# Performance work log

Measured on AMD Instinct MI355X. Metric: run time of the kernel, lower is better.

The kernel has to match this reference:

```python
import jax, jax.numpy as jnp
import numpy as np

B, S, D, H, DFF = 2, 2048, 768, 12, 3072
DK = D // H
EPS = 1e-6
NEG = -1e9


def setup_inputs() -> dict:
    key = jax.random.key(0)
    ks = jax.random.split(key, 16)
    s = 1.0 / np.sqrt(D)
    inp = {
        'x': jax.random.normal(ks[0], (B, S, D), jnp.float32),
        'wq': jax.random.normal(ks[1], (D, D), jnp.float32) * s,
        'bq': jnp.zeros((D,), jnp.float32),
        'wk': jax.random.normal(ks[2], (D, D), jnp.float32) * s,
        'bk': jnp.zeros((D,), jnp.float32),
        'wv': jax.random.normal(ks[3], (D, D), jnp.float32) * s,
        'bv': jnp.zeros((D,), jnp.float32),
        'wo': jax.random.normal(ks[4], (D, D), jnp.float32) * s,
        'bo': jnp.zeros((D,), jnp.float32),
        'w1': jax.random.normal(ks[5], (D, DFF), jnp.float32) * s,
        'b1': jnp.zeros((DFF,), jnp.float32),
        'w2': jax.random.normal(ks[6], (DFF, D), jnp.float32) * (1.0 / np.sqrt(DFF)),
        'b2': jnp.zeros((D,), jnp.float32),
        'alpha1': jnp.ones((1,), jnp.float32),
        'beta1': jnp.zeros((1,), jnp.float32),
        'alpha2': jnp.ones((1,), jnp.float32),
        'beta2': jnp.zeros((1,), jnp.float32),
        'mask': jax.random.randint(ks[7], (1, 1, S, S), 0, 2, jnp.int32),
    }
    return inp


def layernorm(x, alpha, beta):
    # torch: mean and UNBIASED std (ddof=1), eps added to std (not variance)
    mean = jnp.mean(x, axis=-1, keepdims=True)
    std = jnp.std(x, axis=-1, keepdims=True, ddof=1)
    return alpha * (x - mean) / (std + EPS) + beta


def encoder_layer(x, wq, bq, wk, bk, wv, bv, wo, bo, w1, b1, w2, b2,
                  alpha1, beta1, alpha2, beta2, mask):
    # projections -> [B, H, S, DK]
    def split_heads(t):
        return t.reshape(B, S, H, DK).transpose(0, 2, 1, 3)
    q = split_heads(x @ wq + bq)
    k = split_heads(x @ wk + bk)
    v = split_heads(x @ wv + bv)
    scores = jnp.einsum('bhqd,bhkd->bhqk', q, k) / np.sqrt(DK)  # [B,H,S,S]
    scores = jnp.where(mask == 0, NEG, scores)
    attn = jax.nn.softmax(scores, axis=-1)
    ctx = jnp.einsum('bhqk,bhkd->bhqd', attn, v)
    ctx = ctx.transpose(0, 2, 1, 3).reshape(B, S, D)
    attn_out = ctx @ wo + bo
    x = layernorm(x + attn_out, alpha1, beta1)
    ff = jax.nn.relu(x @ w1 + b1) @ w2 + b2
    x = layernorm(x + ff, alpha2, beta2)
    return x


def reference(x, wq, bq, wk, bk, wv, bv, wo, bo, w1, b1, w2, b2,
              alpha1, beta1, alpha2, beta2, mask):
    return encoder_layer(x, wq, bq, wk, bk, wv, bv, wo, bo, w1, b1, w2, b2,
                         alpha1, beta1, alpha2, beta2, mask)
```

## Files before the change

### kernel.cpp

```cpp
#include <hip/hip_runtime.h>
#include <hip/hip_bf16.h>


typedef short short8 __attribute__((ext_vector_type(8)));
typedef float floatx4 __attribute__((ext_vector_type(4)));
typedef unsigned short ushort_t;
typedef ushort_t ushort4_t __attribute__((ext_vector_type(4)));

#define B_ 2
#define S_ 2048
#define D_ 768
#define H_ 12
#define DK_ 64
#define DFF_ 3072
#define M_ (B_ * S_)
#define RS_ (3 * D_)

#define LOG2E 1.44269504f
#define FMAX_SHIFT 16.0f

__device__ __forceinline__ float bf2f(ushort_t h) {
  union { unsigned int u; float f; } v; v.u = ((unsigned int)h) << 16; return v.f;
}
__device__ __forceinline__ ushort_t f2bf(float f) {
  union { float f; unsigned int u; } v; v.f = f;
  unsigned int u = v.u;
  unsigned int r = (u + 0x7fffu + ((u >> 16) & 1u)) >> 16;
  return (ushort_t)r;
}

__global__ __launch_bounds__(256) void transpose_f2b(
    const float* __restrict__ in, ushort_t* __restrict__ out, int K, int N) {
  __shared__ ushort_t t[32][33];
  const int nt = blockIdx.x * 32, kt = blockIdx.y * 32;
  const int tx = threadIdx.x, ty = threadIdx.y;
#pragma unroll
  for (int i = 0; i < 4; i++)
    t[ty + i * 8][tx] = f2bf(in[(size_t)(kt + ty + i * 8) * N + nt + tx]);
  __syncthreads();
#pragma unroll
  for (int i = 0; i < 4; i++)
    out[(size_t)(nt + ty + i * 8) * K + kt + tx] = t[tx][ty + i * 8];
}

__global__ __launch_bounds__(256) void transpose4_f2b(
    const float* __restrict__ wq, const float* __restrict__ wk,
    const float* __restrict__ wv, const float* __restrict__ wo,
    ushort_t* __restrict__ wTqkv, ushort_t* __restrict__ woT) {
  __shared__ ushort_t t[32][33];
  const int z = blockIdx.z;
  const float* in = (z == 0) ? wq : (z == 1) ? wk : (z == 2) ? wv : wo;
  ushort_t* out = (z < 3) ? (wTqkv + (size_t)z * D_ * D_) : woT;
  const int nt = blockIdx.x * 32, kt = blockIdx.y * 32;
  const int tx = threadIdx.x, ty = threadIdx.y;
#pragma unroll
  for (int i = 0; i < 4; i++)
    t[ty + i * 8][tx] = f2bf(in[(size_t)(kt + ty + i * 8) * D_ + nt + tx]);
  __syncthreads();
#pragma unroll
  for (int i = 0; i < 4; i++)
    out[(size_t)(nt + ty + i * 8) * D_ + kt + tx] = t[tx][ty + i * 8];
}

__global__ __launch_bounds__(256) void mask_to_biasp(
    const int* __restrict__ mask, ushort_t* __restrict__ out) {
  const int t = blockIdx.x * 256 + threadIdx.x;
  const int q = t >> 8;
  const int cc = t & 255;
  const int k0 = (cc >> 3) * 64;
  const int g = cc & 7, f = g >> 2, lq = g & 3;
  const int* mrow = mask + (size_t)q * S_ + k0;
  const ushort_t cm = f2bf(-1.4427e9f);
  const ushort_t cu = f2bf(-FMAX_SHIFT * LOG2E);
  short8 o;
#pragma unroll
  for (int n2 = 0; n2 < 2; n2++)
#pragma unroll
    for (int r = 0; r < 4; r++) {
      const int kpl = 32 * f + 16 * n2 + 4 * lq + r;
      o[n2 * 4 + r] = (short)((mrow[kpl] == 0) ? cm : cu);
    }
  *(short8*)(out + (size_t)q * S_ + k0 + g * 8) = o;
}

__global__ __launch_bounds__(256) void vtrans(
    const ushort_t* __restrict__ qkv, ushort_t* __restrict__ vt) {
  __shared__ __align__(16) ushort_t T[64 * 72];
  const int tid = threadIdx.x;
  const int bh = blockIdx.y, b = bh / H_, h = bh % H_;
  const int k0 = blockIdx.x * 64;
  const ushort_t* vbase = qkv + (size_t)(b * S_) * RS_ + 2 * D_ + h * DK_;
#pragma unroll
  for (int i = 0; i < 2; i++) {
    const int idx = tid + i * 256;
    const int r = idx >> 3, c = idx & 7;
    short8 vv = *(const short8*)(vbase + (size_t)(k0 + r) * RS_ + c * 8);
    const int sw = (r >> 3) ^ c;
#pragma unroll
    for (int j = 0; j < 8; j++)
      T[(c * 8 + j) * 72 + sw * 8 + (r & 7)] = (ushort_t)vv[j];
  }
  __syncthreads();
#pragma unroll
  for (int i = 0; i < 2; i++) {
    const int ch = tid + i * 256;
    const int d = ch >> 3, g = ch & 7, f = g >> 2, lq = g & 3;
    short8 o;
#pragma unroll
    for (int n2 = 0; n2 < 2; n2++)
#pragma unroll
      for (int r = 0; r < 4; r++) {
        const int kpl = 32 * f + 16 * n2 + 4 * lq + r;
        o[n2 * 4 + r] = (short)T[d * 72 + (((kpl >> 3) ^ (d >> 3)) * 8) + (kpl & 7)];
      }
    *(short8*)(vt + ((size_t)bh * 64 + d) * S_ + k0 + g * 8) = o;
  }
}

__global__ __launch_bounds__(256) void cvt_f2b(
    const float* __restrict__ in, ushort_t* __restrict__ out, int n) {
  const int i = (blockIdx.x * 256 + threadIdx.x) * 4;
  if (i >= n) return;
#pragma unroll
  for (int j = 0; j < 4; j++) out[i + j] = f2bf(in[i + j]);
}

__global__ void concat3(const float* __restrict__ a, const float* __restrict__ b,
                        const float* __restrict__ c, float* __restrict__ o, int n) {
  int i = blockIdx.x * 256 + threadIdx.x;
  if (i >= 3 * n) return;
  o[i] = (i < n) ? a[i] : (i < 2 * n ? b[i - n] : c[i - 2 * n]);
}

template <int BN>
__global__ __launch_bounds__(256) void gemm_bt_t(
    const ushort_t* __restrict__ A, const ushort_t* __restrict__ Bt,
    const float* __restrict__ bias, ushort_t* __restrict__ C,
    int M, int N, int K, int relu, int qcols, float qscale) {
  constexpr int WN = (BN == 128) ? 2 : 1;
  constexpr int WM = 4 / WN;
  constexpr int FI = 128 / WM / 16;
  constexpr int FJ = BN / WN / 16;
  __shared__ __align__(16) ushort_t Al[128 * 32];
  __shared__ __align__(16) ushort_t Bl[BN * 32];
  const int tid = threadIdx.x;
  const int w = tid >> 6, lane = tid & 63;
  const int wm = (WN == 2) ? (w >> 1) : w;
  const int wn = (WN == 2) ? (w & 1) : 0;
  const int lq = lane >> 4, lr = lane & 15;
  const int m0 = blockIdx.y * 128, n0 = blockIdx.x * BN;

  floatx4 acc[FI][FJ];
#pragma unroll
  for (int i = 0; i < FI; i++)
#pragma unroll
    for (int j = 0; j < FJ; j++) acc[i][j] = (floatx4){0.f, 0.f, 0.f, 0.f};

  for (int k0 = 0; k0 < K; k0 += 32) {
    __syncthreads();
#pragma unroll
    for (int i = 0; i < 2; i++) {
      const int base = (w * 2 + i) * 512;
      const int e = base + lane * 8;
      const int row = e >> 5, col = e & 31;
      __builtin_amdgcn_global_load_lds(
          (const __attribute__((address_space(1))) void*)(A + (size_t)(m0 + row) * K + k0 + col),
          (__attribute__((address_space(3))) void*)(&Al[base]), 16, 0, 0);
    }
#pragma unroll
    for (int i = 0; i < BN / 64; i++) {
      const int base = (w * (BN / 64) + i) * 512;
      const int e = base + lane * 8;
      const int row = e >> 5, col = e & 31;
      __builtin_amdgcn_global_load_lds(
          (const __attribute__((address_space(1))) void*)(Bt + (size_t)(n0 + row) * K + k0 + col),
          (__attribute__((address_space(3))) void*)(&Bl[base]), 16, 0, 0);
    }
    __syncthreads();

    short8 af[FI], bf[FJ];
#pragma unroll
    for (int i = 0; i < FI; i++)
      af[i] = *(const short8*)&Al[(wm * (FI * 16) + i * 16 + lr) * 32 + lq * 8];
#pragma unroll
    for (int j = 0; j < FJ; j++)
      bf[j] = *(const short8*)&Bl[(wn * (FJ * 16) + j * 16 + lr) * 32 + lq * 8];
#pragma unroll
    for (int i = 0; i < FI; i++)
#pragma unroll
      for (int j = 0; j < FJ; j++)
        acc[i][j] = __builtin_amdgcn_mfma_f32_16x16x32_bf16(af[i], bf[j], acc[i][j], 0, 0, 0);
  }

#pragma unroll
  for (int i = 0; i < FI; i++) {
    const int m = m0 + wm * (FI * 16) + i * 16 + lq * 4;
#pragma unroll
    for (int j = 0; j < FJ; j++) {
      const int n = n0 + wn * (FJ * 16) + j * 16 + lr;
      const float bv = bias[n];
#pragma unroll
      for (int r = 0; r < 4; r++) {
        float v = acc[i][j][r] + bv;
        if (n < qcols) v *= qscale;
        if (relu) v = v > 0.f ? v : 0.f;
        C[(size_t)(m + r) * N + n] = f2bf(v);
      }
    }
  }
}

__global__ __launch_bounds__(256, 3) void flash_attn(
    const ushort_t* __restrict__ qkv, const ushort_t* __restrict__ vt,
    const ushort_t* __restrict__ maskp, ushort_t* __restrict__ ctx) {
  __shared__ __align__(16) ushort_t lds[2][3][64 * 64];
  const int tid = threadIdx.x;
  const int w = tid >> 6, lane = tid & 63;
  const int lq = lane >> 4, lr = lane & 15;
  const int blk = blockIdx.x;
  const int bh = blk >> 5, qb = blk & 31;
  const int b = bh / H_, h = bh % H_;
  const int q0 = qb * 64;
  const ushort_t* qbase = qkv + (size_t)(b * S_) * RS_ + h * DK_;
  const ushort_t* kbase = qbase + D_;
  const ushort_t* vtb   = vt + (size_t)bh * DK_ * S_;
  const ushort_t* mb    = maskp + (size_t)q0 * S_;

  short8 qfr[2];
#pragma unroll
  for (int f = 0; f < 2; f++)
    qfr[f] = *(const short8*)(
        qbase + (size_t)(q0 + w * 16 + lr) * RS_ + f * 32 + lq * 8);

  auto stage = [&](int k0, int s) {
#pragma unroll
    for (int i = 0; i < 2; i++) {
      const int id = i * 256 + tid;
      const int row = id >> 3;
      const int cc = ((id & 7) ^ (row & 7)) * 8;
      const int dbase = (i * 256 + w * 64) * 8;
      __builtin_amdgcn_global_load_lds(
          (const __attribute__((address_space(1))) void*)(kbase + (size_t)(k0 + row) * RS_ + cc),
          (__attribute__((address_space(3))) void*)(&lds[s][0][dbase]), 16, 0, 0);
      __builtin_amdgcn_global_load_lds(
          (const __attribute__((address_space(1))) void*)(vtb + (size_t)row * S_ + k0 + cc),
          (__attribute__((address_space(3))) void*)(&lds[s][1][dbase]), 16, 0, 0);
      __builtin_amdgcn_global_load_lds(
          (const __attribute__((address_space(1))) void*)(mb + (size_t)row * S_ + k0 + cc),
          (__attribute__((address_space(3))) void*)(&lds[s][2][dbase]), 16, 0, 0);
    }
  };

  floatx4 oacc[4];
#pragma unroll
  for (int dt = 0; dt < 4; dt++) oacc[dt] = (floatx4){0.f, 0.f, 0.f, 0.f};
  float li = 0.f;

  stage(0, 0);
  __syncthreads();

  const int sw8 = lr & 7;
  const int c0 = (lq ^ sw8) * 8;
  const int c1 = ((4 + lq) ^ sw8) * 8;

  for (int t = 0; t < S_ / 64; t++) {
    const int s = t & 1;
    stage((t + 1) * 64, s ^ 1);

    const ushort_t* kl = &lds[s][0][0];
    const ushort_t* vl = &lds[s][1][0];
    const ushort_t* ml = &lds[s][2][0];

    const int mrow = (w * 16 + lr) * 64;
    short8 bb0 = *(const short8*)(ml + mrow + c0);
    short8 bb1 = *(const short8*)(ml + mrow + c1);

    floatx4 sacc[4];
#pragma unroll
    for (int n = 0; n < 4; n++) sacc[n] = (floatx4){0.f, 0.f, 0.f, 0.f};
#pragma unroll
    for (int n = 0; n < 4; n++) {
      const int krow = (n * 16 + lr) * 64;
      short8 a0 = *(const short8*)(kl + krow + c0);
      short8 a1 = *(const short8*)(kl + krow + c1);
      sacc[n] = __builtin_amdgcn_mfma_f32_16x16x32_bf16(a0, qfr[0], sacc[n], 0, 0, 0);
      sacc[n] = __builtin_amdgcn_mfma_f32_16x16x32_bf16(a1, qfr[1], sacc[n], 0, 0, 0);
    }

    short8 pf[2];
#pragma unroll
    for (int f = 0; f < 2; f++) {
      const short8 bb = f ? bb1 : bb0;
      union { __hip_bfloat162 h2[4]; short8 v; } u;
#pragma unroll
      for (int jj = 0; jj < 4; jj++) {
        const int e0 = jj * 2, e1 = jj * 2 + 1;
        float2 p2;
        p2.x = __builtin_amdgcn_exp2f(sacc[2 * f + (e0 >> 2)][e0 & 3] + bf2f((ushort_t)bb[e0]));
        p2.y = __builtin_amdgcn_exp2f(sacc[2 * f + (e1 >> 2)][e1 & 3] + bf2f((ushort_t)bb[e1]));
        li += p2.x + p2.y;
        u.h2[jj] = __float22bfloat162_rn(p2);
      }
      pf[f] = u.v;
    }

#pragma unroll
    for (int dt = 0; dt < 4; dt++) {
      const int vrow = (dt * 16 + lr) * 64;
      short8 v0 = *(const short8*)(vl + vrow + c0);
      short8 v1 = *(const short8*)(vl + vrow + c1);
      oacc[dt] = __builtin_amdgcn_mfma_f32_16x16x32_bf16(v0, pf[0], oacc[dt], 0, 0, 0);
      oacc[dt] = __builtin_amdgcn_mfma_f32_16x16x32_bf16(v1, pf[1], oacc[dt], 0, 0, 0);
    }
    __syncthreads();
  }

  li += __shfl_xor(li, 16);
  li += __shfl_xor(li, 32);
  const float inv = 1.f / (li + 1e-37f);

  const size_t row = (size_t)(b * S_ + q0 + w * 16 + lr) * D_ + h * DK_;
#pragma unroll
  for (int dt = 0; dt < 4; dt++) {
    ushort4_t o;
#pragma unroll
    for (int r = 0; r < 4; r++) o[r] = f2bf(oacc[dt][r] * inv);
    *(ushort4_t*)(ctx + row + dt * 16 + lq * 4) = o;
  }
}

template <bool XF, bool OF>
__global__ __launch_bounds__(256) void add_ln(
    const void* __restrict__ xv, const ushort_t* __restrict__ y,
    const float* __restrict__ alpha, const float* __restrict__ beta,
    void* __restrict__ outv) {
  const int row = blockIdx.x, tid = threadIdx.x;
  const int w = tid >> 6, lane = tid & 63;
  __shared__ float red[8];
  const ushort_t* yr = y + (size_t)row * D_;
  float v[3];
#pragma unroll
  for (int i = 0; i < 3; i++) {
    const int c = tid + i * 256;
    float xv_;
    if (XF) xv_ = ((const float*)xv)[(size_t)row * D_ + c];
    else    xv_ = bf2f(((const ushort_t*)xv)[(size_t)row * D_ + c]);
    v[i] = xv_ + bf2f(yr[c]);
  }
  float s = v[0] + v[1] + v[2];
#pragma unroll
  for (int off = 1; off < 64; off <<= 1) s += __shfl_xor(s, off);
  if (lane == 0) red[w] = s;
  __syncthreads();
  const float mean = (red[0] + red[1] + red[2] + red[3]) / (float)D_;
  float d = 0.f;
#pragma unroll
  for (int i = 0; i < 3; i++) { const float t = v[i] - mean; d += t * t; }
#pragma unroll
  for (int off = 1; off < 64; off <<= 1) d += __shfl_xor(d, off);
  if (lane == 0) red[4 + w] = d;
  __syncthreads();
  const float var = (red[4] + red[5] + red[6] + red[7]) / (float)(D_ - 1);
  const float inv = 1.f / (sqrtf(var) + 1e-6f);
  const float a = alpha[0] * inv, bt = beta[0];
#pragma unroll
  for (int i = 0; i < 3; i++) {
    const int c = tid + i * 256;
    const float o = a * (v[i] - mean) + bt;
    if (OF) ((float*)outv)[(size_t)row * D_ + c] = o;
    else    ((ushort_t*)outv)[(size_t)row * D_ + c] = f2bf(o);
  }
}

extern "C" void kernel_launch(void* const* d_in, const int* in_sizes, int n_in,
                              void* d_out, int out_size, void* d_ws, size_t ws_size,
                              hipStream_t stream) {
  const float* x   = (const float*)d_in[0];
  const float* wq  = (const float*)d_in[1];
  const float* bq  = (const float*)d_in[2];
  const float* wk  = (const float*)d_in[3];
  const float* bk  = (const float*)d_in[4];
  const float* wv  = (const float*)d_in[5];
  const float* bv  = (const float*)d_in[6];
  const float* wo  = (const float*)d_in[7];
  const float* bo  = (const float*)d_in[8];
  const float* w1  = (const float*)d_in[9];
  const float* b1  = (const float*)d_in[10];
  const float* w2  = (const float*)d_in[11];
  const float* b2  = (const float*)d_in[12];
  const float* a1  = (const float*)d_in[13];
  const float* be1 = (const float*)d_in[14];
  const float* a2  = (const float*)d_in[15];
  const float* be2 = (const float*)d_in[16];
  const int*   msk = (const int*)d_in[17];

  const size_t E_xb    = 0;
  const size_t E_wTqkv = E_xb    + (size_t)M_ * D_;
  const size_t E_woT   = E_wTqkv + (size_t)3 * D_ * D_;
  const size_t E_w1T   = E_woT   + (size_t)D_ * D_;
  const size_t E_w2T   = E_w1T   + (size_t)DFF_ * D_;
  const size_t E_bqkv  = E_w2T   + (size_t)D_ * DFF_;
  const size_t E_qkv   = E_bqkv  + (size_t)2 * 3 * D_;
  const size_t E_ctx   = E_qkv   + (size_t)M_ * 3 * D_;
  const size_t E_attn  = E_ctx   + (size_t)M_ * D_;
  const size_t E_x1    = E_attn  + (size_t)M_ * D_;
  const size_t E_h1    = E_x1    + (size_t)M_ * D_;
  const size_t E_ff    = E_h1    + (size_t)M_ * DFF_;
  const size_t E_total = E_ff    + (size_t)M_ * D_;
  if (ws_size < E_total * sizeof(ushort_t)) return;

  ushort_t* ws    = (ushort_t*)d_ws;
  ushort_t* xb    = ws + E_xb;
  ushort_t* wTqkv = ws + E_wTqkv;
  ushort_t* woT   = ws + E_woT;
  ushort_t* w1T   = ws + E_w1T;
  ushort_t* w2T   = ws + E_w2T;
  float*    bqkv  = (float*)(ws + E_bqkv);
  ushort_t* qkv   = ws + E_qkv;
  ushort_t* ctx   = ws + E_ctx;
  ushort_t* attn  = ws + E_attn;
  ushort_t* x1    = ws + E_x1;
  ushort_t* h1    = ws + E_h1;
  ushort_t* maskp = ws + E_h1;
  ushort_t* vt    = ws + E_h1 + (size_t)S_ * S_;
  ushort_t* ff    = ws + E_ff;

  const float SCALE_Q = 0.125f * LOG2E;

  const dim3 tb(32, 8);
  transpose4_f2b<<<dim3(24, 24, 4), tb, 0, stream>>>(wq, wk, wv, wo, wTqkv, woT);
  transpose_f2b<<<dim3(96, 24), tb, 0, stream>>>(w1, w1T, D_, DFF_);
  transpose_f2b<<<dim3(24, 96), tb, 0, stream>>>(w2, w2T, DFF_, D_);
  mask_to_biasp<<<(S_ * S_ / 8) / 256, 256, 0, stream>>>(msk, maskp);
  concat3<<<9, 256, 0, stream>>>(bq, bk, bv, bqkv, D_);
  cvt_f2b<<<(M_ * D_ / 4 + 255) / 256, 256, 0, stream>>>(x, xb, M_ * D_);

  gemm_bt_t<128><<<dim3(18, 32), 256, 0, stream>>>(xb, wTqkv, bqkv, qkv,
                                                   M_, 3 * D_, D_, 0, D_, SCALE_Q);
  vtrans<<<dim3(S_ / 64, B_ * H_), 256, 0, stream>>>(qkv, vt);
  flash_attn<<<(B_ * H_) * (S_ / 64), 256, 0, stream>>>(qkv, vt, maskp, ctx);
  gemm_bt_t<64><<<dim3(12, 32), 256, 0, stream>>>(ctx, woT, bo, attn,
                                                  M_, D_, D_, 0, 0, 1.f);
  add_ln<true, false><<<M_, 256, 0, stream>>>(x, attn, a1, be1, x1);
  gemm_bt_t<128><<<dim3(24, 32), 256, 0, stream>>>(x1, w1T, b1, h1,
                                                   M_, DFF_, D_, 1, 0, 1.f);
  gemm_bt_t<64><<<dim3(12, 32), 256, 0, stream>>>(h1, w2T, b2, ff,
                                                  M_, D_, DFF_, 0, 0, 1.f);
  add_ln<false, true><<<M_, 256, 0, stream>>>(x1, ff, a2, be2, d_out);
}
```

Measured before the change: 333.0 us.

## Double-buffer GEMM LDS tiles and split-K the D-output GEMMs with fused reduction

The GEMM kernel now double-buffers its LDS tiles and issues the next K-tile's global-to-LDS loads before computing the current one, so loads overlap the MFMA work. The two GEMMs with N=768 (output projection and FFN down-projection) switch to split-K over two halves. They write fp32 partials, and the add+layernorm kernel sums the partials and adds the bias. The QKV GEMM uses 64-wide tiles to launch more blocks. This targets low occupancy (384 blocks) and load latency, at the cost of extra fp32 partial traffic and reuse of workspace regions for the partials.

Result: faster. 309.9 us (-7.0%).

```diff
diff --git a/kernel.cpp b/kernel.cpp
--- a/kernel.cpp
+++ b/kernel.cpp
@@ -132,17 +132,17 @@
   o[i] = (i < n) ? a[i] : (i < 2 * n ? b[i - n] : c[i - 2 * n]);
 }
 
-template <int BN>
+template <int BN, bool SPLIT>
 __global__ __launch_bounds__(256) void gemm_bt_t(
     const ushort_t* __restrict__ A, const ushort_t* __restrict__ Bt,
-    const float* __restrict__ bias, ushort_t* __restrict__ C,
+    const float* __restrict__ bias, void* __restrict__ Cv,
     int M, int N, int K, int relu, int qcols, float qscale) {
   constexpr int WN = (BN == 128) ? 2 : 1;
   constexpr int WM = 4 / WN;
   constexpr int FI = 128 / WM / 16;
   constexpr int FJ = BN / WN / 16;
-  __shared__ __align__(16) ushort_t Al[128 * 32];
-  __shared__ __align__(16) ushort_t Bl[BN * 32];
+  __shared__ __align__(16) ushort_t Al[2][128 * 32];
+  __shared__ __align__(16) ushort_t Bl[2][BN * 32];
   const int tid = threadIdx.x;
   const int w = tid >> 6, lane = tid & 63;
   const int wm = (WN == 2) ? (w >> 1) : w;
@@ -150,14 +150,12 @@
   const int lq = lane >> 4, lr = lane & 15;
   const int m0 = blockIdx.y * 128, n0 = blockIdx.x * BN;
 
-  floatx4 acc[FI][FJ];
-#pragma unroll
-  for (int i = 0; i < FI; i++)
-#pragma unroll
-    for (int j = 0; j < FJ; j++) acc[i][j] = (floatx4){0.f, 0.f, 0.f, 0.f};
-
-  for (int k0 = 0; k0 < K; k0 += 32) {
-    __syncthreads();
+  int kBeg = 0, kEnd = K;
+  if (SPLIT) { const int half = K >> 1; kBeg = blockIdx.z * half; kEnd = kBeg + half; }
+  const int NT = (kEnd - kBeg) / 32;
+
+  auto stage = [&](int kt, int s) {
+    const int k0 = kBeg + kt * 32;
 #pragma unroll
     for (int i = 0; i < 2; i++) {
       const int base = (w * 2 + i) * 512;
@@ -165,7 +163,7 @@
       const int row = e >> 5, col = e & 31;
       __builtin_amdgcn_global_load_lds(
           (const __attribute__((address_space(1))) void*)(A + (size_t)(m0 + row) * K + k0 + col),
-          (__attribute__((address_space(3))) void*)(&Al[base]), 16, 0, 0);
+          (__attribute__((address_space(3))) void*)(&Al[s][base]), 16, 0, 0);
     }
 #pragma unroll
     for (int i = 0; i < BN / 64; i++) {
@@ -174,17 +172,29 @@
       const int row = e >> 5, col = e & 31;
       __builtin_amdgcn_global_load_lds(
           (const __attribute__((address_space(1))) void*)(Bt + (size_t)(n0 + row) * K + k0 + col),
-          (__attribute__((address_space(3))) void*)(&Bl[base]), 16, 0, 0);
-    }
+          (__attribute__((address_space(3))) void*)(&Bl[s][base]), 16, 0, 0);
+    }
+  };
+
+  floatx4 acc[FI][FJ];
+#pragma unroll
+  for (int i = 0; i < FI; i++)
+#pragma unroll
+    for (int j = 0; j < FJ; j++) acc[i][j] = (floatx4){0.f, 0.f, 0.f, 0.f};
+
+  stage(0, 0);
+  for (int kt = 0; kt < NT; kt++) {
+    const int s = kt & 1;
     __syncthreads();
+    if (kt + 1 < NT) stage(kt + 1, s ^ 1);
 
     short8 af[FI], bf[FJ];
 #pragma unroll
     for (int i = 0; i < FI; i++)
-      af[i] = *(const short8*)&Al[(wm * (FI * 16) + i * 16 + lr) * 32 + lq * 8];
+      af[i] = *(const short8*)&Al[s][(wm * (FI * 16) + i * 16 + lr) * 32 + lq * 8];
 #pragma unroll
     for (int j = 0; j < FJ; j++)
-      bf[j] = *(const short8*)&Bl[(wn * (FJ * 16) + j * 16 + lr) * 32 + lq * 8];
+      bf[j] = *(const short8*)&Bl[s][(wn * (FJ * 16) + j * 16 + lr) * 32 + lq * 8];
 #pragma unroll
     for (int i = 0; i < FI; i++)
 #pragma unroll
@@ -198,13 +208,20 @@
 #pragma unroll
     for (int j = 0; j < FJ; j++) {
       const int n = n0 + wn * (FJ * 16) + j * 16 + lr;
-      const float bv = bias[n];
-#pragma unroll
-      for (int r = 0; r < 4; r++) {
-        float v = acc[i][j][r] + bv;
-        if (n < qcols) v *= qscale;
-        if (relu) v = v > 0.f ? v : 0.f;
-        C[(size_t)(m + r) * N + n] = f2bf(v);
+      if (SPLIT) {
+        float* P = (float*)Cv + (size_t)blockIdx.z * M * N;
+#pragma unroll
+        for (int r = 0; r < 4; r++)
+          P[(size_t)(m + r) * N + n] = acc[i][j][r];
+      } else {
+        const float bv = bias[n];
+#pragma unroll
+        for (int r = 0; r < 4; r++) {
+          float v = acc[i][j][r] + bv;
+          if (n < qcols) v *= qscale;
+          if (relu) v = v > 0.f ? v : 0.f;
+          ((ushort_t*)Cv)[(size_t)(m + r) * N + n] = f2bf(v);
+        }
       }
     }
   }
@@ -330,22 +347,23 @@
 }
 
 template <bool XF, bool OF>
-__global__ __launch_bounds__(256) void add_ln(
-    const void* __restrict__ xv, const ushort_t* __restrict__ y,
+__global__ __launch_bounds__(256) void add_ln_comb(
+    const void* __restrict__ xv, const float* __restrict__ P0,
+    const float* __restrict__ P1, const float* __restrict__ cb,
     const float* __restrict__ alpha, const float* __restrict__ beta,
     void* __restrict__ outv) {
   const int row = blockIdx.x, tid = threadIdx.x;
   const int w = tid >> 6, lane = tid & 63;
   __shared__ float red[8];
-  const ushort_t* yr = y + (size_t)row * D_;
   float v[3];
 #pragma unroll
   for (int i = 0; i < 3; i++) {
     const int c = tid + i * 256;
+    const size_t idx = (size_t)row * D_ + c;
     float xv_;
-    if (XF) xv_ = ((const float*)xv)[(size_t)row * D_ + c];
-    else    xv_ = bf2f(((const ushort_t*)xv)[(size_t)row * D_ + c]);
-    v[i] = xv_ + bf2f(yr[c]);
+    if (XF) xv_ = ((const float*)xv)[idx];
+    else    xv_ = bf2f(((const ushort_t*)xv)[idx]);
+    v[i] = xv_ + (P0[idx] + P1[idx] + cb[c]);
   }
   float s = v[0] + v[1] + v[2];
 #pragma unroll
@@ -418,12 +436,12 @@
   float*    bqkv  = (float*)(ws + E_bqkv);
   ushort_t* qkv   = ws + E_qkv;
   ushort_t* ctx   = ws + E_ctx;
-  ushort_t* attn  = ws + E_attn;
   ushort_t* x1    = ws + E_x1;
   ushort_t* h1    = ws + E_h1;
   ushort_t* maskp = ws + E_h1;
   ushort_t* vt    = ws + E_h1 + (size_t)S_ * S_;
-  ushort_t* ff    = ws + E_ff;
+  float*    Pattn = (float*)(ws + E_h1);
+  float*    Pff2  = (float*)(ws + E_qkv);
 
   const float SCALE_Q = 0.125f * LOG2E;
 
@@ -435,16 +453,18 @@
   concat3<<<9, 256, 0, stream>>>(bq, bk, bv, bqkv, D_);
   cvt_f2b<<<(M_ * D_ / 4 + 255) / 256, 256, 0, stream>>>(x, xb, M_ * D_);
 
-  gemm_bt_t<128><<<dim3(18, 32), 256, 0, stream>>>(xb, wTqkv, bqkv, qkv,
-                                                   M_, 3 * D_, D_, 0, D_, SCALE_Q);
+  gemm_bt_t<64, false><<<dim3(36, 32), 256, 0, stream>>>(
+      xb, wTqkv, bqkv, qkv, M_, 3 * D_, D_, 0, D_, SCALE_Q);
   vtrans<<<dim3(S_ / 64, B_ * H_), 256, 0, stream>>>(qkv, vt);
   flash_attn<<<(B_ * H_) * (S_ / 64), 256, 0, stream>>>(qkv, vt, maskp, ctx);
-  gemm_bt_t<64><<<dim3(12, 32), 256, 0, stream>>>(ctx, woT, bo, attn,
-                                                  M_, D_, D_, 0, 0, 1.f);
-  add_ln<true, false><<<M_, 256, 0, stream>>>(x, attn, a1, be1, x1);
-  gemm_bt_t<128><<<dim3(24, 32), 256, 0, stream>>>(x1, w1T, b1, h1,
-                                                   M_, DFF_, D_, 1, 0, 1.f);
-  gemm_bt_t<64><<<dim3(12, 32), 256, 0, stream>>>(h1, w2T, b2, ff,
-                                                  M_, D_, DFF_, 0, 0, 1.f);
-  add_ln<false, true><<<M_, 256, 0, stream>>>(x1, ff, a2, be2, d_out);
-}
+  gemm_bt_t<64, true><<<dim3(12, 32, 2), 256, 0, stream>>>(
+      ctx, woT, nullptr, Pattn, M_, D_, D_, 0, 0, 1.f);
+  add_ln_comb<true, false><<<M_, 256, 0, stream>>>(
+      x, Pattn, Pattn + (size_t)M_ * D_, bo, a1, be1, x1);
+  gemm_bt_t<128, false><<<dim3(24, 32), 256, 0, stream>>>(
+      x1, w1T, b1, h1, M_, DFF_, D_, 1, 0, 1.f);
+  gemm_bt_t<64, true><<<dim3(12, 32, 2), 256, 0, stream>>>(
+      h1, w2T, nullptr, Pff2, M_, D_, DFF_, 0, 0, 1.f);
+  add_ln_comb<false, true><<<M_, 256, 0, stream>>>(
+      x1, Pff2, Pff2 + (size_t)M_ * D_, b2, a2, be2, d_out);
+}
```
